# Kernel optimization log

Hardware: AMD Instinct MI355X
Metric: run time of the kernel (lower is better)

Reference implementation:

```python
import jax, jax.numpy as jnp
import numpy as np

D_K = 64

def setup_inputs() -> dict:
    key = jax.random.key(0)
    k1, k2, k3, k4 = jax.random.split(key, 4)
    hidden_states = jax.random.normal(k1, (2, 16, 128, 16, 16), dtype=jnp.float32)
    # nn.Linear(hidden, d, bias=False); stored as [in, out] for x @ W
    w_q = jax.random.normal(k2, (128, 64), dtype=jnp.float32) * 0.05
    w_k = jax.random.normal(k3, (128, 64), dtype=jnp.float32) * 0.05
    w_v = jax.random.normal(k4, (128, 64), dtype=jnp.float32) * 0.05
    return {"hidden_states": hidden_states, "w_q": w_q, "w_k": w_k, "w_v": w_v}

def reference(hidden_states, w_q, w_k, w_v):
    # (B, T, C, H, W) -> (B, T, H, W, C) -> (N, C)
    x = jnp.transpose(hidden_states, (0, 1, 3, 4, 2))
    x = x.reshape(-1, x.shape[-1])                      # [N, C], N = B*T*H*W
    q = x @ w_q                                          # [N, d_k]
    k = x @ w_k                                          # [N, d_k]
    v = x @ w_v                                          # [N, d_v]
    scores = (q @ k.T) / jnp.sqrt(jnp.asarray(D_K, x.dtype))  # [N, N]
    attn = jax.nn.softmax(scores, axis=1)                # softmax over dim=1
    out = attn @ v                                       # [N, d_v]
    return out
```

## Files before the change

kernel.cpp:

```cpp
#include <hip/hip_runtime.h>
#include <hip/hip_bf16.h>

typedef float f32x4 __attribute__((ext_vector_type(4)));
typedef short bf16x8 __attribute__((ext_vector_type(8)));

#define MFMA32 __builtin_amdgcn_mfma_f32_16x16x32_bf16

__device__ __forceinline__ unsigned short f2bf(float f) {
  union { float f; unsigned u; } v; v.f = f;
  unsigned u = v.u;
  u += 0x7FFFu + ((u >> 16) & 1u);
  return (unsigned short)(u >> 16);
}

__device__ __forceinline__ bf16x8 pack8_bf16(float a, float b, float c, float d,
                                             float e, float f, float g, float h) {
  union { bf16x8 v; __hip_bfloat162 p[4]; } u;
  u.p[0] = __float22bfloat162_rn(make_float2(a, b));
  u.p[1] = __float22bfloat162_rn(make_float2(c, d));
  u.p[2] = __float22bfloat162_rn(make_float2(e, f));
  u.p[3] = __float22bfloat162_rn(make_float2(g, h));
  return u.v;
}

__device__ __forceinline__ void stage16(const unsigned short* gbase,
                                        unsigned short* lbase, int lane) {
#if __has_builtin(__builtin_amdgcn_global_load_lds)
  __builtin_amdgcn_global_load_lds(
      (const __attribute__((address_space(1))) void*)(gbase + lane * 8),
      (__attribute__((address_space(3))) void*)lbase, 16, 0, 0);
#else
  *(bf16x8*)(lbase + lane * 8) = *(const bf16x8*)(gbase + lane * 8);
#endif
}

__global__ __launch_bounds__(256) void qkv_kernel(
    const float* __restrict__ hs,
    const float* __restrict__ wq, const float* __restrict__ wk,
    const float* __restrict__ wv,
    unsigned short* __restrict__ qb, unsigned short* __restrict__ kpack,
    unsigned short* __restrict__ vpack)
{
  __shared__ __align__(16) float Wl[128 * 64];
  __shared__ float xs[32 * 129];
  const int t = threadIdx.x;
  const int mat = blockIdx.y;
  const float* __restrict__ W = (mat == 0) ? wq : (mat == 1) ? wk : wv;
  #pragma unroll
  for (int i = 0; i < 8; ++i) {
    *(f32x4*)(Wl + i * 1024 + t * 4) = *(const f32x4*)(W + i * 1024 + t * 4);
  }
  const int n0 = blockIdx.x * 32;
  const int bt = n0 >> 8;
  const int sp0 = n0 & 255;
  {
    const float* __restrict__ src = hs + (size_t)bt * 32768 + sp0;
    const int s = t & 31, cb = t >> 5;
    #pragma unroll
    for (int i = 0; i < 16; ++i) {
      const int c = i * 8 + cb;
      xs[s * 129 + c] = src[c * 256 + s];
    }
  }
  __syncthreads();
  const int s = t & 31, g = t >> 5;
  float acc[8];
  #pragma unroll
  for (int j = 0; j < 8; ++j) acc[j] = 0.f;
  #pragma unroll 4
  for (int c = 0; c < 128; ++c) {
    const float xv = xs[s * 129 + c];
    const f32x4 w0 = *(const f32x4*)(Wl + c * 64 + g * 8);
    const f32x4 w1 = *(const f32x4*)(Wl + c * 64 + g * 8 + 4);
    acc[0] += xv * w0[0]; acc[1] += xv * w0[1];
    acc[2] += xv * w0[2]; acc[3] += xv * w0[3];
    acc[4] += xv * w1[0]; acc[5] += xv * w1[1];
    acc[6] += xv * w1[2]; acc[7] += xv * w1[3];
  }
  const int n = n0 + s;
  const float SCALE = 1.4426950408889634f / 8.0f;
  if (mat == 0) {
    #pragma unroll
    for (int j = 0; j < 8; ++j) qb[n * 64 + g * 8 + j] = f2bf(acc[j] * SCALE);
  } else if (mat == 1) {
    const int kvb32 = n >> 5, kvl = n & 31;
    const int ti = (kvl >> 2) & 1;
    const int lowk = ((kvl >> 3) << 2) | (kvl & 3);
    const int h = g >> 2, quadk = g & 3;
    unsigned short* dst =
        kpack + (((size_t)(kvb32 * 2 + ti) * 2 + h) * 64 + quadk * 16 + lowk) * 8;
    #pragma unroll
    for (int j = 0; j < 8; ++j) dst[j] = f2bf(acc[j]);
  } else {
    const int kvb32 = n >> 5, kvl = n & 31;
    const int quadv = kvl >> 3, jj = kvl & 7;
    #pragma unroll
    for (int jw = 0; jw < 8; ++jw) {
      const int d = g * 8 + jw, dt = d >> 4, lowd = d & 15;
      vpack[(((size_t)kvb32 * 4 + dt) * 64 + quadv * 16 + lowd) * 8 + jj] =
          f2bf(acc[jw]);
    }
  }
}

__global__ __launch_bounds__(256, 2) void flash_kernel(
    const unsigned short* __restrict__ qb,
    const unsigned short* __restrict__ kpack,
    const unsigned short* __restrict__ vpack,
    float* __restrict__ opart, float* __restrict__ lpart, int kvlen)
{
  __shared__ __align__(16) unsigned short Kl[2][4][2048];
  __shared__ __align__(16) unsigned short Vl[2][4][2048];
  const int t = threadIdx.x;
  const int w = t >> 6, lane = t & 63;
  const int quad = lane >> 4, low = lane & 15;
  const int bid = blockIdx.x;
  const int q0 = (bid & 31) * 256 + w * 64;
  const int g = bid >> 5;
  const int kvb32_0 = (g * kvlen) >> 5;
  const int nch = kvlen >> 7;

  bf16x8 bq[4][2];
  #pragma unroll
  for (int qt = 0; qt < 4; ++qt)
    #pragma unroll
    for (int h = 0; h < 2; ++h)
      bq[qt][h] = *(const bf16x8*)(qb + (q0 + qt * 16 + low) * 64 + h * 32 + quad * 8);

  f32x4 O[4][4];
  f32x4 O4[4];
  #pragma unroll
  for (int qt = 0; qt < 4; ++qt) {
    #pragma unroll
    for (int dt = 0; dt < 4; ++dt) O[qt][dt] = (f32x4){0.f, 0.f, 0.f, 0.f};
    O4[qt] = (f32x4){0.f, 0.f, 0.f, 0.f};
  }
  const bf16x8 ones = {16256, 16256, 16256, 16256, 16256, 16256, 16256, 16256};

  #define STAGE_CHUNK(b, c)                                                   \
    {                                                                         \
      const size_t kb = (size_t)(kvb32_0 + (c) * 4 + w) * 2048;               \
      _Pragma("unroll")                                                       \
      for (int r = 0; r < 4; ++r) {                                           \
        stage16(kpack + kb + r * 512, &Kl[b][w][r * 512], lane);              \
        stage16(vpack + kb + r * 512, &Vl[b][w][r * 512], lane);              \
      }                                                                       \
    }

  STAGE_CHUNK(0, 0)
  __syncthreads();

  for (int c = 0; c < nch; ++c) {
    const int b = c & 1;
    if (c + 1 < nch) STAGE_CHUNK(b ^ 1, c + 1)
    #pragma unroll
    for (int j = 0; j < 4; ++j) {
      bf16x8 kf[4], vf[4];
      #pragma unroll
      for (int f = 0; f < 4; ++f)
        kf[f] = *(const bf16x8*)&Kl[b][j][f * 512 + lane * 8];
      #pragma unroll
      for (int f = 0; f < 4; ++f)
        vf[f] = *(const bf16x8*)&Vl[b][j][f * 512 + lane * 8];
      #pragma unroll
      for (int qt = 0; qt < 4; ++qt) {
        f32x4 SA = {0.f, 0.f, 0.f, 0.f}, SB = {0.f, 0.f, 0.f, 0.f};
        SA = MFMA32(kf[0], bq[qt][0], SA, 0, 0, 0);
        SA = MFMA32(kf[1], bq[qt][1], SA, 0, 0, 0);
        SB = MFMA32(kf[2], bq[qt][0], SB, 0, 0, 0);
        SB = MFMA32(kf[3], bq[qt][1], SB, 0, 0, 0);
        const float pa0 = __builtin_amdgcn_exp2f(SA[0]);
        const float pa1 = __builtin_amdgcn_exp2f(SA[1]);
        const float pa2 = __builtin_amdgcn_exp2f(SA[2]);
        const float pa3 = __builtin_amdgcn_exp2f(SA[3]);
        const float pb0 = __builtin_amdgcn_exp2f(SB[0]);
        const float pb1 = __builtin_amdgcn_exp2f(SB[1]);
        const float pb2 = __builtin_amdgcn_exp2f(SB[2]);
        const float pb3 = __builtin_amdgcn_exp2f(SB[3]);
        const bf16x8 pf = pack8_bf16(pa0, pa1, pa2, pa3, pb0, pb1, pb2, pb3);
        #pragma unroll
        for (int dt = 0; dt < 4; ++dt)
          O[qt][dt] = MFMA32(vf[dt], pf, O[qt][dt], 0, 0, 0);
        O4[qt] = MFMA32(ones, pf, O4[qt], 0, 0, 0);
      }
    }
    __syncthreads();
  }

  #pragma unroll
  for (int qt = 0; qt < 4; ++qt) {
    const size_t qrow = (size_t)g * 8192 + q0 + qt * 16;
    #pragma unroll
    for (int dt = 0; dt < 4; ++dt)
      *(f32x4*)(opart + (qrow + low) * 64 + dt * 16 + quad * 4) = O[qt][dt];
    if (quad == 0) lpart[qrow + low] = O4[qt][0];
  }
}

__global__ __launch_bounds__(256) void reduce_kernel(
    const float* __restrict__ opart, const float* __restrict__ lpart,
    float* __restrict__ out, int G)
{
  const int idx = blockIdx.x * 256 + threadIdx.x;
  const int q = idx >> 4;
  const int d4 = (idx & 15) * 4;
  float den = 0.f;
  f32x4 num = {0.f, 0.f, 0.f, 0.f};
  for (int g = 0; g < G; ++g) {
    den += lpart[g * 8192 + q];
    const f32x4 o = *(const f32x4*)(opart + ((size_t)g * 8192 + q) * 64 + d4);
    num[0] += o[0]; num[1] += o[1]; num[2] += o[2]; num[3] += o[3];
  }
  const float r = 1.0f / den;
  f32x4 res = {num[0] * r, num[1] * r, num[2] * r, num[3] * r};
  *(f32x4*)(out + (size_t)q * 64 + d4) = res;
}

extern "C" void kernel_launch(void* const* d_in, const int* in_sizes, int n_in,
                              void* d_out, int out_size, void* d_ws, size_t ws_size,
                              hipStream_t stream) {
  const float* hs = (const float*)d_in[0];
  const float* wq = (const float*)d_in[1];
  const float* wk = (const float*)d_in[2];
  const float* wv = (const float*)d_in[3];
  float* out = (float*)d_out;
  char* ws = (char*)d_ws;

  unsigned short* qb    = (unsigned short*)ws;
  unsigned short* kpack = (unsigned short*)(ws + (1 << 20));
  unsigned short* vpack = (unsigned short*)(ws + (2 << 20));

  int G = 16;
  {
    const size_t per_g = (size_t)8192 * 64 * 4 + (size_t)8192 * 4;
    while (G > 1 && ws_size < (size_t)(3 << 20) + (size_t)G * per_g) G >>= 1;
  }
  float* opart = (float*)(ws + (3 << 20));
  float* lpart = (float*)(ws + (3 << 20) + (size_t)G * 8192 * 64 * 4);

  qkv_kernel<<<dim3(256, 3, 1), 256, 0, stream>>>(hs, wq, wk, wv, qb, kpack, vpack);
  flash_kernel<<<32 * G, 256, 0, stream>>>(qb, kpack, vpack, opart, lpart, 8192 / G);
  reduce_kernel<<<512, 256, 0, stream>>>(opart, lpart, out, G);
}
```

Measured before the change: 98.28 us.

## Double KV split count, halve flash chunk, store bf16 partials, fuse QKV projection blocks

```diff
diff --git a/kernel.cpp b/kernel.cpp
--- a/kernel.cpp
+++ b/kernel.cpp
@@ -3,6 +3,7 @@
 
 typedef float f32x4 __attribute__((ext_vector_type(4)));
 typedef short bf16x8 __attribute__((ext_vector_type(8)));
+typedef short bf16x4 __attribute__((ext_vector_type(4)));
 
 #define MFMA32 __builtin_amdgcn_mfma_f32_16x16x32_bf16
 
@@ -20,6 +21,13 @@
   u.p[1] = __float22bfloat162_rn(make_float2(c, d));
   u.p[2] = __float22bfloat162_rn(make_float2(e, f));
   u.p[3] = __float22bfloat162_rn(make_float2(g, h));
+  return u.v;
+}
+
+__device__ __forceinline__ bf16x4 pack4_bf16(float a, float b, float c, float d) {
+  union { bf16x4 v; __hip_bfloat162 p[2]; } u;
+  u.p[0] = __float22bfloat162_rn(make_float2(a, b));
+  u.p[1] = __float22bfloat162_rn(make_float2(c, d));
   return u.v;
 }
 
@@ -44,12 +52,6 @@
   __shared__ __align__(16) float Wl[128 * 64];
   __shared__ float xs[32 * 129];
   const int t = threadIdx.x;
-  const int mat = blockIdx.y;
-  const float* __restrict__ W = (mat == 0) ? wq : (mat == 1) ? wk : wv;
-  #pragma unroll
-  for (int i = 0; i < 8; ++i) {
-    *(f32x4*)(Wl + i * 1024 + t * 4) = *(const f32x4*)(W + i * 1024 + t * 4);
-  }
   const int n0 = blockIdx.x * 32;
   const int bt = n0 >> 8;
   const int sp0 = n0 & 255;
@@ -62,55 +64,66 @@
       xs[s * 129 + c] = src[c * 256 + s];
     }
   }
-  __syncthreads();
   const int s = t & 31, g = t >> 5;
-  float acc[8];
-  #pragma unroll
-  for (int j = 0; j < 8; ++j) acc[j] = 0.f;
-  #pragma unroll 4
-  for (int c = 0; c < 128; ++c) {
-    const float xv = xs[s * 129 + c];
-    const f32x4 w0 = *(const f32x4*)(Wl + c * 64 + g * 8);
-    const f32x4 w1 = *(const f32x4*)(Wl + c * 64 + g * 8 + 4);
-    acc[0] += xv * w0[0]; acc[1] += xv * w0[1];
-    acc[2] += xv * w0[2]; acc[3] += xv * w0[3];
-    acc[4] += xv * w1[0]; acc[5] += xv * w1[1];
-    acc[6] += xv * w1[2]; acc[7] += xv * w1[3];
-  }
   const int n = n0 + s;
   const float SCALE = 1.4426950408889634f / 8.0f;
-  if (mat == 0) {
-    #pragma unroll
-    for (int j = 0; j < 8; ++j) qb[n * 64 + g * 8 + j] = f2bf(acc[j] * SCALE);
-  } else if (mat == 1) {
-    const int kvb32 = n >> 5, kvl = n & 31;
-    const int ti = (kvl >> 2) & 1;
-    const int lowk = ((kvl >> 3) << 2) | (kvl & 3);
-    const int h = g >> 2, quadk = g & 3;
-    unsigned short* dst =
-        kpack + (((size_t)(kvb32 * 2 + ti) * 2 + h) * 64 + quadk * 16 + lowk) * 8;
-    #pragma unroll
-    for (int j = 0; j < 8; ++j) dst[j] = f2bf(acc[j]);
-  } else {
-    const int kvb32 = n >> 5, kvl = n & 31;
-    const int quadv = kvl >> 3, jj = kvl & 7;
-    #pragma unroll
-    for (int jw = 0; jw < 8; ++jw) {
-      const int d = g * 8 + jw, dt = d >> 4, lowd = d & 15;
-      vpack[(((size_t)kvb32 * 4 + dt) * 64 + quadv * 16 + lowd) * 8 + jj] =
-          f2bf(acc[jw]);
-    }
-  }
-}
-
-__global__ __launch_bounds__(256, 2) void flash_kernel(
+
+  #pragma unroll 1
+  for (int mat = 0; mat < 3; ++mat) {
+    const float* __restrict__ W = (mat == 0) ? wq : (mat == 1) ? wk : wv;
+    __syncthreads();
+    #pragma unroll
+    for (int i = 0; i < 8; ++i)
+      *(f32x4*)(Wl + i * 1024 + t * 4) = *(const f32x4*)(W + i * 1024 + t * 4);
+    __syncthreads();
+
+    float acc[8];
+    #pragma unroll
+    for (int j = 0; j < 8; ++j) acc[j] = 0.f;
+    #pragma unroll 4
+    for (int c = 0; c < 128; ++c) {
+      const float xv = xs[s * 129 + c];
+      const f32x4 w0 = *(const f32x4*)(Wl + c * 64 + g * 8);
+      const f32x4 w1 = *(const f32x4*)(Wl + c * 64 + g * 8 + 4);
+      acc[0] += xv * w0[0]; acc[1] += xv * w0[1];
+      acc[2] += xv * w0[2]; acc[3] += xv * w0[3];
+      acc[4] += xv * w1[0]; acc[5] += xv * w1[1];
+      acc[6] += xv * w1[2]; acc[7] += xv * w1[3];
+    }
+
+    if (mat == 0) {
+      #pragma unroll
+      for (int j = 0; j < 8; ++j) qb[n * 64 + g * 8 + j] = f2bf(acc[j] * SCALE);
+    } else if (mat == 1) {
+      const int kvb32 = n >> 5, kvl = n & 31;
+      const int ti = (kvl >> 2) & 1;
+      const int lowk = ((kvl >> 3) << 2) | (kvl & 3);
+      const int h = g >> 2, quadk = g & 3;
+      unsigned short* dst =
+          kpack + (((size_t)(kvb32 * 2 + ti) * 2 + h) * 64 + quadk * 16 + lowk) * 8;
+      #pragma unroll
+      for (int j = 0; j < 8; ++j) dst[j] = f2bf(acc[j]);
+    } else {
+      const int kvb32 = n >> 5, kvl = n & 31;
+      const int quadv = kvl >> 3, jj = kvl & 7;
+      #pragma unroll
+      for (int jw = 0; jw < 8; ++jw) {
+        const int d = g * 8 + jw, dt = d >> 4, lowd = d & 15;
+        vpack[(((size_t)kvb32 * 4 + dt) * 64 + quadv * 16 + lowd) * 8 + jj] =
+            f2bf(acc[jw]);
+      }
+    }
+  }
+}
+
+__global__ __launch_bounds__(256, 3) void flash_kernel(
     const unsigned short* __restrict__ qb,
     const unsigned short* __restrict__ kpack,
     const unsigned short* __restrict__ vpack,
-    float* __restrict__ opart, float* __restrict__ lpart, int kvlen)
+    unsigned short* __restrict__ opart, float* __restrict__ lpart, int kvlen)
 {
-  __shared__ __align__(16) unsigned short Kl[2][4][2048];
-  __shared__ __align__(16) unsigned short Vl[2][4][2048];
+  __shared__ __align__(16) unsigned short Kl[2][2][2048];
+  __shared__ __align__(16) unsigned short Vl[2][2][2048];
   const int t = threadIdx.x;
   const int w = t >> 6, lane = t & 63;
   const int quad = lane >> 4, low = lane & 15;
@@ -118,7 +131,7 @@
   const int q0 = (bid & 31) * 256 + w * 64;
   const int g = bid >> 5;
   const int kvb32_0 = (g * kvlen) >> 5;
-  const int nch = kvlen >> 7;
+  const int nch = kvlen >> 6;
 
   bf16x8 bq[4][2];
   #pragma unroll
@@ -139,11 +152,12 @@
 
   #define STAGE_CHUNK(b, c)                                                   \
     {                                                                         \
-      const size_t kb = (size_t)(kvb32_0 + (c) * 4 + w) * 2048;               \
+      const int jj = w >> 1, f0 = (w & 1) * 2;                                \
+      const size_t base = (size_t)(kvb32_0 + (c) * 2 + jj) * 2048;            \
       _Pragma("unroll")                                                       \
-      for (int r = 0; r < 4; ++r) {                                           \
-        stage16(kpack + kb + r * 512, &Kl[b][w][r * 512], lane);              \
-        stage16(vpack + kb + r * 512, &Vl[b][w][r * 512], lane);              \
+      for (int r = 0; r < 2; ++r) {                                           \
+        stage16(kpack + base + (f0 + r) * 512, &Kl[b][jj][(f0 + r) * 512], lane); \
+        stage16(vpack + base + (f0 + r) * 512, &Vl[b][jj][(f0 + r) * 512], lane); \
       }                                                                       \
     }
 
@@ -154,7 +168,7 @@
     const int b = c & 1;
     if (c + 1 < nch) STAGE_CHUNK(b ^ 1, c + 1)
     #pragma unroll
-    for (int j = 0; j < 4; ++j) {
+    for (int j = 0; j < 2; ++j) {
       bf16x8 kf[4], vf[4];
       #pragma unroll
       for (int f = 0; f < 4; ++f)
@@ -191,14 +205,17 @@
   for (int qt = 0; qt < 4; ++qt) {
     const size_t qrow = (size_t)g * 8192 + q0 + qt * 16;
     #pragma unroll
-    for (int dt = 0; dt < 4; ++dt)
-      *(f32x4*)(opart + (qrow + low) * 64 + dt * 16 + quad * 4) = O[qt][dt];
+    for (int dt = 0; dt < 4; ++dt) {
+      const bf16x4 ob =
+          pack4_bf16(O[qt][dt][0], O[qt][dt][1], O[qt][dt][2], O[qt][dt][3]);
+      *(bf16x4*)(opart + (qrow + low) * 64 + dt * 16 + quad * 4) = ob;
+    }
     if (quad == 0) lpart[qrow + low] = O4[qt][0];
   }
 }
 
 __global__ __launch_bounds__(256) void reduce_kernel(
-    const float* __restrict__ opart, const float* __restrict__ lpart,
+    const unsigned short* __restrict__ opart, const float* __restrict__ lpart,
     float* __restrict__ out, int G)
 {
   const int idx = blockIdx.x * 256 + threadIdx.x;
@@ -208,8 +225,11 @@
   f32x4 num = {0.f, 0.f, 0.f, 0.f};
   for (int g = 0; g < G; ++g) {
     den += lpart[g * 8192 + q];
-    const f32x4 o = *(const f32x4*)(opart + ((size_t)g * 8192 + q) * 64 + d4);
-    num[0] += o[0]; num[1] += o[1]; num[2] += o[2]; num[3] += o[3];
+    const ushort4 o = *(const ushort4*)(opart + ((size_t)g * 8192 + q) * 64 + d4);
+    union { unsigned u; float f; } c0, c1, c2, c3;
+    c0.u = (unsigned)o.x << 16; c1.u = (unsigned)o.y << 16;
+    c2.u = (unsigned)o.z << 16; c3.u = (unsigned)o.w << 16;
+    num[0] += c0.f; num[1] += c1.f; num[2] += c2.f; num[3] += c3.f;
   }
   const float r = 1.0f / den;
   f32x4 res = {num[0] * r, num[1] * r, num[2] * r, num[3] * r};
@@ -230,15 +250,15 @@
   unsigned short* kpack = (unsigned short*)(ws + (1 << 20));
   unsigned short* vpack = (unsigned short*)(ws + (2 << 20));
 
-  int G = 16;
+  int G = 32;
   {
-    const size_t per_g = (size_t)8192 * 64 * 4 + (size_t)8192 * 4;
+    const size_t per_g = (size_t)8192 * 64 * 2 + (size_t)8192 * 4;
     while (G > 1 && ws_size < (size_t)(3 << 20) + (size_t)G * per_g) G >>= 1;
   }
-  float* opart = (float*)(ws + (3 << 20));
-  float* lpart = (float*)(ws + (3 << 20) + (size_t)G * 8192 * 64 * 4);
-
-  qkv_kernel<<<dim3(256, 3, 1), 256, 0, stream>>>(hs, wq, wk, wv, qb, kpack, vpack);
+  unsigned short* opart = (unsigned short*)(ws + (3 << 20));
+  float* lpart = (float*)(ws + (3 << 20) + (size_t)G * 8192 * 64 * 2);
+
+  qkv_kernel<<<256, 256, 0, stream>>>(hs, wq, wk, wv, qb, kpack, vpack);
   flash_kernel<<<32 * G, 256, 0, stream>>>(qb, kpack, vpack, opart, lpart, 8192 / G);
   reduce_kernel<<<512, 256, 0, stream>>>(opart, lpart, out, G);
 }
```

Result: slower. 119.1 us (+21.2%).
